# Performance work log

Hardware: AMD Instinct MI355X
Metric: run time of the kernel (lower is better)

The kernel has to match this reference:

```python
import jax, jax.numpy as jnp
import numpy as np

EMBED_DIM = 2048
NUM_HEADS = 16
HEAD_DIM = EMBED_DIM // NUM_HEADS
WINDOW = 512  # window_size; also used as chunk size (S must be a multiple)


def setup_inputs() -> dict:
    key = jax.random.key(0)
    k1, k2, k3 = jax.random.split(key, 3)
    B, S = 2, 4096
    x = jax.random.normal(k1, (B, S, EMBED_DIM), dtype=jnp.float32)
    w_qkv = jax.random.normal(k2, (3 * EMBED_DIM, EMBED_DIM), dtype=jnp.float32) * 0.02
    w_out = jax.random.normal(k3, (EMBED_DIM, EMBED_DIM), dtype=jnp.float32) * 0.02
    return {"x": x, "w_qkv": w_qkv, "w_out": w_out}


def _sliding_window_attn(q, k, v, window):
    # q,k,v: [B,H,S,d]; causal sliding window: kv valid iff 0 <= q_idx - kv_idx <= window.
    # Chunked O(S*window): each query chunk of size C=window attends to its own
    # chunk and the previous one (exactly covers the band of width window+1).
    B, H, S, d = q.shape
    C = window
    nc = S // C
    qc = q.reshape(B, H, nc, C, d)

    def two_chunks(t):
        tc = t.reshape(B, H, nc, C, d)
        prev = jnp.pad(tc[:, :, :-1], ((0, 0), (0, 0), (1, 0), (0, 0), (0, 0)))
        return jnp.concatenate([prev, tc], axis=3)  # [B,H,nc,2C,d]

    kc = two_chunks(k)
    vc = two_chunks(v)

    scale = 1.0 / np.sqrt(d).astype(np.float32)
    scores = jnp.einsum('bhnid,bhnjd->bhnij', qc, kc) * scale  # [B,H,nc,C,2C]

    i = jnp.arange(C)[:, None]            # local query index
    j = jnp.arange(2 * C)[None, :]        # local kv index within the 2-chunk span
    band = (j >= i) & (j <= i + C)        # causal & within window (C == window)
    kv_global = (jnp.arange(nc)[:, None, None] - 1) * C + j[None]  # [nc,1,2C]
    mask = band[None] & (kv_global >= 0)  # [nc,C,2C]; drops padded chunk 0 keys

    scores = jnp.where(mask[None, None], scores, jnp.finfo(scores.dtype).min)
    probs = jax.nn.softmax(scores, axis=-1)
    out = jnp.einsum('bhnij,bhnjd->bhnid', probs, vc)  # [B,H,nc,C,d]
    return out.reshape(B, H, S, d)


def reference(x, w_qkv, w_out):
    B, S, E = x.shape
    qkv = jnp.einsum('bse,fe->bsf', x, w_qkv)                       # [B,S,3E]
    qkv = qkv.reshape(B, S, 3, NUM_HEADS, HEAD_DIM)
    qkv = jnp.transpose(qkv, (2, 0, 3, 1, 4))                        # [3,B,H,S,d]
    q, k, v = qkv[0], qkv[1], qkv[2]
    attn = _sliding_window_attn(q, k, v, WINDOW)                     # [B,H,S,d]
    attn = jnp.transpose(attn, (0, 2, 1, 3)).reshape(B, S, E)
    return jnp.einsum('bse,fe->bsf', attn, w_out)
```

## Files before the change

### kernel.cpp

```cpp
#include <hip/hip_runtime.h>
#include <hip/hip_bf16.h>
#include <math.h>


#define SEQ   4096
#define BATCH 2
#define EMBED 2048
#define HEADS 16
#define HDIM  128
#define NELEM (BATCH * SEQ * EMBED)
#define SCL2E (0.088388347648318447f * 1.4426950408889634f)

typedef __attribute__((ext_vector_type(8))) short short8;
typedef __attribute__((ext_vector_type(4))) float f32x4;

__device__ __forceinline__ unsigned short f2bf(float f) {
    unsigned int u = __float_as_uint(f);
    u = (u + 0x7fff + ((u >> 16) & 1)) >> 16;
    return (unsigned short)u;
}

__device__ __forceinline__ unsigned int cvt_pk_bf16(float a, float b) {
    unsigned int r;
    asm volatile("v_cvt_pk_bf16_f32 %0, %1, %2" : "=v"(r) : "v"(a), "v"(b));
    return r;
}

__global__ void cast3_kernel(const float* __restrict__ x,
                             const float* __restrict__ wq,
                             const float* __restrict__ wo,
                             unsigned short* __restrict__ xb,
                             unsigned short* __restrict__ wqb,
                             unsigned short* __restrict__ wob)
{
    const int nx = NELEM / 8;
    const int nq = 3 * EMBED * EMBED / 8;
    const int no = EMBED * EMBED / 8;
    int i = blockIdx.x * blockDim.x + threadIdx.x;
    const float* s;
    unsigned short* d;
    int j;
    if (i < nx)                { s = x;  d = xb;  j = i; }
    else if (i < nx + nq)      { s = wq; d = wqb; j = i - nx; }
    else if (i < nx + nq + no) { s = wo; d = wob; j = i - nx - nq; }
    else return;
    const float4 v0 = ((const float4*)s)[2 * j];
    const float4 v1 = ((const float4*)s)[2 * j + 1];
    union { unsigned short us[8]; uint4 u4; } o;
    o.us[0] = f2bf(v0.x); o.us[1] = f2bf(v0.y); o.us[2] = f2bf(v0.z); o.us[3] = f2bf(v0.w);
    o.us[4] = f2bf(v1.x); o.us[5] = f2bf(v1.y); o.us[6] = f2bf(v1.z); o.us[7] = f2bf(v1.w);
    ((uint4*)d)[j] = o.u4;
}

template <int MODE>
__global__ __launch_bounds__(512)
void gemm256_kernel(const unsigned short* __restrict__ A,
                    const unsigned short* __restrict__ B,
                    float* __restrict__ C,
                    unsigned short* __restrict__ P0,
                    unsigned short* __restrict__ P1,
                    int M, int N, int K)
{
    __shared__ __align__(16) char lds[131072];

    const int tid  = threadIdx.x;
    const int lane = tid & 63;
    const int w    = tid >> 6;
    const int wm   = w >> 2;
    const int wn   = w & 3;
    const int l16  = lane & 15;
    const int kg   = lane >> 4;

    const int nwg  = gridDim.x * gridDim.y;
    const int bidl = blockIdx.y * gridDim.x + blockIdx.x;
    const int cpx  = nwg >> 3;
    const int swzb = (bidl & 7) * cpx + (bidl >> 3);
    const int m0   = (swzb / gridDim.x) * 256;
    const int n0   = (swzb % gridDim.x) * 256;

    const int srow = w * 8 + (lane >> 3);
    const int sch8 = ((lane & 7) ^ (lane >> 3)) * 8;

    auto stage = [&](const unsigned short* X, int rowbase, int t2, int ldsbase) {
#pragma unroll
        for (int u = 0; u < 2; ++u) {
            const unsigned short* g = X + (size_t)(rowbase + u * 64 + srow) * K
                                      + t2 * 64 + sch8;
            unsigned int lb = __builtin_amdgcn_readfirstlane(
                (unsigned int)(uintptr_t)(lds + ldsbase + u * 8192 + w * 1024));
            asm volatile("s_mov_b32 m0, %0\n\t"
                         "global_load_lds_dwordx4 %1, off"
                         :: "s"(lb), "v"(g) : "memory");
        }
    };
    auto rdA = [&](int p, int mf, int ks) -> short8 {
        return *(const short8*)(lds + p * 32768 + (wm * 128 + mf * 16 + l16) * 128
                                + (((ks * 4 + kg) ^ (l16 & 7)) << 4));
    };
    auto rdB = [&](int p, int nf, int ks) -> short8 {
        return *(const short8*)(lds + 65536 + p * 32768
                                + (wn * 64 + nf * 16 + l16) * 128
                                + (((ks * 4 + kg) ^ (l16 & 7)) << 4));
    };

    f32x4 acc[8][4];
#pragma unroll
    for (int i = 0; i < 8; ++i)
#pragma unroll
        for (int j = 0; j < 4; ++j) acc[i][j] = (f32x4)0.f;

    const int NT = K >> 6;

    stage(A, m0 + 0,   0, 0);
    stage(A, m0 + 128, 0, 16384);
    stage(B, n0 + 0,   0, 65536);
    stage(B, n0 + 128, 0, 65536 + 16384);
    __syncthreads();

    for (int t = 0; t < NT; ++t) {
        const int p = t & 1;
        if (t + 1 < NT) {
            stage(A, m0 + 0,   t + 1, (p ^ 1) * 32768);
            stage(A, m0 + 128, t + 1, (p ^ 1) * 32768 + 16384);
            stage(B, n0 + 0,   t + 1, 65536 + (p ^ 1) * 32768);
            stage(B, n0 + 128, t + 1, 65536 + (p ^ 1) * 32768 + 16384);
        }
        short8 bfr[4][2];
#pragma unroll
        for (int nf = 0; nf < 4; ++nf)
#pragma unroll
            for (int ks = 0; ks < 2; ++ks) bfr[nf][ks] = rdB(p, nf, ks);
#pragma unroll
        for (int mf = 0; mf < 8; ++mf) {
            const short8 a0 = rdA(p, mf, 0);
            const short8 a1 = rdA(p, mf, 1);
#pragma unroll
            for (int nf = 0; nf < 4; ++nf) {
                acc[mf][nf] = __builtin_amdgcn_mfma_f32_16x16x32_bf16(
                    a0, bfr[nf][0], acc[mf][nf], 0, 0, 0);
                acc[mf][nf] = __builtin_amdgcn_mfma_f32_16x16x32_bf16(
                    a1, bfr[nf][1], acc[mf][nf], 0, 0, 0);
            }
        }
        __syncthreads();
    }

    if (MODE == 1) {
        const int cb = n0 + wn * 64;
        unsigned short* dst = (cb >> 11) ? P1 : P0;
        const int h  = (cb >> 7) & 15;
        const int db = cb & 127;
#pragma unroll
        for (int fi = 0; fi < 8; ++fi)
#pragma unroll
            for (int r = 0; r < 4; ++r) {
                const int mrow = m0 + wm * 128 + fi * 16 + kg * 4 + r;
                const int b = mrow >> 12, s = mrow & 4095;
                unsigned short* drow = dst + ((size_t)((b << 4) + h) * SEQ + s) * HDIM
                                       + db + l16;
#pragma unroll
                for (int nf = 0; nf < 4; ++nf) drow[nf * 16] = f2bf(acc[fi][nf][r]);
            }
    } else if (MODE == 2) {
#pragma unroll
        for (int fi = 0; fi < 8; ++fi)
#pragma unroll
            for (int r = 0; r < 4; ++r) {
                const int mrow = m0 + wm * 128 + fi * 16 + kg * 4 + r;
                const int h = mrow >> 7, d = mrow & 127;
#pragma unroll
                for (int nf = 0; nf < 4; ++nf) {
                    const int col = n0 + wn * 64 + nf * 16 + l16;
                    const int b = col >> 12, s = col & 4095;
                    const int sl = s & 63;
                    const int c = (sl & 0x23) | ((sl & 0x0C) << 1) | ((sl & 0x10) >> 2);
                    P0[((size_t)((b << 4) + h) * HDIM + d) * SEQ + (s & ~63) + c] =
                        f2bf(acc[fi][nf][r]);
                }
            }
    } else {
#pragma unroll
        for (int fi = 0; fi < 8; ++fi)
#pragma unroll
            for (int r = 0; r < 4; ++r) {
                float* crow = C + (size_t)(m0 + wm * 128 + fi * 16 + kg * 4 + r) * N
                              + n0 + wn * 64 + l16;
#pragma unroll
                for (int nf = 0; nf < 4; ++nf) crow[nf * 16] = acc[fi][nf][r];
            }
    }
}

__global__ __launch_bounds__(512)
void swa_mfma_kernel(const unsigned short* __restrict__ Qg,
                     const unsigned short* __restrict__ Kg,
                     const unsigned short* __restrict__ Vtg,
                     unsigned short* __restrict__ O )
{
    __shared__ __align__(16) char lds[65536];

    const int bid = blockIdx.x;
    const int qt  = bid & 31;
    const int h   = (bid >> 5) & 15;
    const int b   = bid >> 9;
    const int q0  = qt * 128;
    const int tid  = threadIdx.x;
    const int w    = tid >> 6;
    const int lane = tid & 63;
    const int l16  = lane & 15;
    const int kg   = lane >> 4;
    const size_t base = (size_t)((b << 4) + h) * SEQ * HDIM;
    const int gq = q0 + w * 16 + l16;

    short8 qf[4];
#pragma unroll
    for (int kw = 0; kw < 4; ++kw)
        qf[kw] = *(const short8*)(Qg + base + (size_t)gq * HDIM + kw * 32 + kg * 8);

    f32x4 acc_o[8];
#pragma unroll
    for (int db = 0; db < 8; ++db) acc_o[db] = (f32x4)0.f;
    float m = -1e30f, l = 0.f;

    auto stageKV = [&](int kt, int buf) {
        const int gk0 = q0 - 512 + kt * 64;
#pragma unroll
        for (int u = 0; u < 2; ++u) {
            {
                const int id  = u * 512 + w * 64 + lane;
                const int row = id >> 4, ch = id & 15;
                const char* g = (const char*)(Kg + base + (size_t)(gk0 + row) * HDIM
                                              + ((ch ^ (row & 7)) << 3));
                unsigned int lb = __builtin_amdgcn_readfirstlane(
                    (unsigned int)(uintptr_t)(lds + buf * 32768 + u * 8192 + w * 1024));
                asm volatile("s_mov_b32 m0, %0\n\t"
                             "global_load_lds_dwordx4 %1, off"
                             :: "s"(lb), "v"(g) : "memory");
            }
            {
                const int id  = u * 512 + w * 64 + lane;
                const int d   = id >> 3, ch = id & 7;
                const char* g = (const char*)(Vtg + base + (size_t)d * SEQ + gk0
                                              + ((ch ^ (d & 7)) << 3));
                unsigned int lb = __builtin_amdgcn_readfirstlane(
                    (unsigned int)(uintptr_t)(lds + buf * 32768 + 16384
                                              + u * 8192 + w * 1024));
                asm volatile("s_mov_b32 m0, %0\n\t"
                             "global_load_lds_dwordx4 %1, off"
                             :: "s"(lb), "v"(g) : "memory");
            }
        }
    };

    const int kt_start = (qt < 4) ? (8 - 2 * qt) : 0;
    stageKV(kt_start, 0);
    int cur = 0;

    for (int kt = kt_start; kt < 10; ++kt) {
        asm volatile("s_waitcnt vmcnt(0)" ::: "memory");
        __syncthreads();
        if (kt + 1 < 10) stageKV(kt + 1, cur ^ 1);

        const int gk0 = q0 - 512 + kt * 64;
        const char* ldsb = lds + cur * 32768;
        const int qlo = q0 + w * 16;
        const bool active = (gk0 <= qlo + 15) && (gk0 + 63 >= qlo - 512);
        if (active) {
            const int dqw = qlo - gk0;
            bool kbok[4];
#pragma unroll
            for (int kb = 0; kb < 4; ++kb)
                kbok[kb] = (kb * 16 <= dqw + 15) && (kb * 16 + 15 >= dqw - 512);

            f32x4 s4[4];
#pragma unroll
            for (int kb = 0; kb < 4; ++kb) s4[kb] = (f32x4)0.f;
#pragma unroll
            for (int kb = 0; kb < 4; ++kb) {
                if (kbok[kb]) {
#pragma unroll
                    for (int kw = 0; kw < 4; ++kw) {
                        short8 kf = *(const short8*)(ldsb + (kb * 16 + l16) * 256
                                                     + (((kw * 4 + kg) ^ (l16 & 7)) << 4));
                        s4[kb] = __builtin_amdgcn_mfma_f32_16x16x32_bf16(
                            kf, qf[kw], s4[kb], 0, 0, 0);
                    }
                }
            }

            const int dq = gq - gk0;
            float p[4][4];
            float tm = -1e30f;
#pragma unroll
            for (int kb = 0; kb < 4; ++kb)
#pragma unroll
                for (int r = 0; r < 4; ++r) {
                    const int koff = kb * 16 + kg * 4 + r;
                    const bool valid = (koff <= dq) && (koff >= dq - 512);
                    const float sv = valid ? s4[kb][r] * SCL2E : -1e30f;
                    p[kb][r] = sv;
                    tm = fmaxf(tm, sv);
                }
            tm = fmaxf(tm, __shfl_xor(tm, 16));
            tm = fmaxf(tm, __shfl_xor(tm, 32));
            const float mn   = fmaxf(m, tm);
            const float corr = __builtin_amdgcn_exp2f(m - mn);
            m = mn;
            l *= corr;
            float cr[4];
#pragma unroll
            for (int r = 0; r < 4; ++r) cr[r] = __shfl(corr, kg * 4 + r);
#pragma unroll
            for (int db = 0; db < 8; ++db)
#pragma unroll
                for (int r = 0; r < 4; ++r) acc_o[db][r] *= cr[r];

            float ts = 0.f;
#pragma unroll
            for (int kb = 0; kb < 4; ++kb)
#pragma unroll
                for (int r = 0; r < 4; ++r) {
                    const float pv = (p[kb][r] > -1e29f)
                                         ? __builtin_amdgcn_exp2f(p[kb][r] - m) : 0.f;
                    p[kb][r] = pv;
                    ts += pv;
                }
            ts += __shfl_xor(ts, 16);
            ts += __shfl_xor(ts, 32);
            l += ts;

            unsigned int dw[4][2];
#pragma unroll
            for (int kb = 0; kb < 4; ++kb) {
                dw[kb][0] = cvt_pk_bf16(p[kb][0], p[kb][1]);
                dw[kb][1] = cvt_pk_bf16(p[kb][2], p[kb][3]);
            }
#pragma unroll
            for (int w2 = 0; w2 < 2; ++w2) {
                if (!(kbok[2 * w2] || kbok[2 * w2 + 1])) continue;
                union { unsigned int u[4]; short8 v; } pu;
                pu.u[0] = dw[2 * w2][0];     pu.u[1] = dw[2 * w2][1];
                pu.u[2] = dw[2 * w2 + 1][0]; pu.u[3] = dw[2 * w2 + 1][1];
#pragma unroll
                for (int db = 0; db < 8; ++db) {
                    short8 vf = *(const short8*)(ldsb + 16384 + (db * 16 + l16) * 128
                                                 + (((w2 * 4 + kg) ^ (l16 & 7)) << 4));
                    acc_o[db] = __builtin_amdgcn_mfma_f32_16x16x32_bf16(
                        pu.v, vf, acc_o[db], 0, 0, 0);
                }
            }
        }
        cur ^= 1;
    }

    const float inv = 1.0f / l;
    float li[4];
#pragma unroll
    for (int r = 0; r < 4; ++r) li[r] = __shfl(inv, kg * 4 + r);
#pragma unroll
    for (int db = 0; db < 8; ++db)
#pragma unroll
        for (int r = 0; r < 4; ++r) {
            const int gqr = q0 + w * 16 + kg * 4 + r;
            O[((size_t)b * SEQ + gqr) * EMBED + h * HDIM + db * 16 + l16] =
                f2bf(acc_o[db][r] * li[r]);
        }
}

extern "C" void kernel_launch(void* const* d_in, const int* in_sizes, int n_in,
                              void* d_out, int out_size, void* d_ws, size_t ws_size,
                              hipStream_t stream)
{
    const float* x     = (const float*)d_in[0];
    const float* w_qkv = (const float*)d_in[1];
    const float* w_out = (const float*)d_in[2];
    float* out = (float*)d_out;

    char* ws = (char*)d_ws;
    unsigned short* xb    = (unsigned short*)(ws);
    unsigned short* wqkvb = (unsigned short*)(ws + 33554432);
    unsigned short* woutb = (unsigned short*)(ws + 58720256);
    unsigned short* qb    = (unsigned short*)(ws + 67108864);
    unsigned short* kb    = (unsigned short*)(ws + 100663296);
    unsigned short* vtb   = (unsigned short*)(ws + 134217728);
    unsigned short* attnb = (unsigned short*)(ws + 167772160);

    const int M = BATCH * SEQ;
    dim3 blk(256);

    hipLaunchKernelGGL(cast3_kernel, dim3(16384), blk, 0, stream,
                       x, w_qkv, w_out, xb, wqkvb, woutb);

    hipLaunchKernelGGL((gemm256_kernel<1>), dim3(16, 32), dim3(512), 0, stream,
                       xb, wqkvb, (float*)nullptr, qb, kb, M, 2 * EMBED, EMBED);

    hipLaunchKernelGGL((gemm256_kernel<2>), dim3(32, 8), dim3(512), 0, stream,
                       wqkvb + (size_t)2 * EMBED * EMBED, xb, (float*)nullptr,
                       vtb, (unsigned short*)nullptr, EMBED, M, EMBED);

    hipLaunchKernelGGL(swa_mfma_kernel, dim3(BATCH * HEADS * (SEQ / 128)), dim3(512),
                       0, stream, qb, kb, vtb, attnb);

    hipLaunchKernelGGL((gemm256_kernel<0>), dim3(8, 32), dim3(512), 0, stream,
                       attnb, woutb, out, (unsigned short*)nullptr,
                       (unsigned short*)nullptr, M, EMBED, EMBED);
}
```

Measured before the change: 332.6 us.

## Merge QK and V projection GEMMs into one launch; widen attention tiles to 256 queries

The QK projection and the transposed V projection are merged into a single launch of 768 workgroups, with the block index selecting the mode. This removes one kernel launch and the tail bubble between the two GEMMs. The sliding-window attention kernel now processes 256 queries per block with 1024 threads instead of 128 with 512, so each staged K/V tile is reused by twice as many query rows and the halo overhead shrinks. In exchange there are fewer, larger attention blocks, which can lower occupancy and shorten the pipeline at the sequence start.

```diff
diff --git a/kernel.cpp b/kernel.cpp
--- a/kernel.cpp
+++ b/kernel.cpp
@@ -52,16 +52,15 @@
     ((uint4*)d)[j] = o.u4;
 }
 
-template <int MODE>
 __global__ __launch_bounds__(512)
-void gemm256_kernel(const unsigned short* __restrict__ A,
-                    const unsigned short* __restrict__ B,
-                    float* __restrict__ C,
-                    unsigned short* __restrict__ P0,
-                    unsigned short* __restrict__ P1,
-                    int M, int N, int K)
+void gemm_proj_kernel(const unsigned short* __restrict__ xb,
+                      const unsigned short* __restrict__ wqkvb,
+                      unsigned short* __restrict__ Qo,
+                      unsigned short* __restrict__ Ko,
+                      unsigned short* __restrict__ Vt)
 {
     __shared__ __align__(16) char lds[131072];
+    const int K = EMBED;
 
     const int tid  = threadIdx.x;
     const int lane = tid & 63;
@@ -71,12 +70,18 @@
     const int l16  = lane & 15;
     const int kg   = lane >> 4;
 
-    const int nwg  = gridDim.x * gridDim.y;
-    const int bidl = blockIdx.y * gridDim.x + blockIdx.x;
+    const int blk   = blockIdx.x;
+    const int mode  = (blk < 512) ? 1 : 2;
+    const int bidl  = (mode == 1) ? blk : blk - 512;
+    const int gx    = (mode == 1) ? 16 : 32;
+    const int nwg   = (mode == 1) ? 512 : 256;
+    const unsigned short* A = (mode == 1) ? xb : (wqkvb + (size_t)2 * EMBED * EMBED);
+    const unsigned short* B = (mode == 1) ? wqkvb : xb;
+
     const int cpx  = nwg >> 3;
     const int swzb = (bidl & 7) * cpx + (bidl >> 3);
-    const int m0   = (swzb / gridDim.x) * 256;
-    const int n0   = (swzb % gridDim.x) * 256;
+    const int m0   = (swzb / gx) * 256;
+    const int n0   = (swzb % gx) * 256;
 
     const int srow = w * 8 + (lane >> 3);
     const int sch8 = ((lane & 7) ^ (lane >> 3)) * 8;
@@ -145,9 +150,9 @@
         __syncthreads();
     }
 
-    if (MODE == 1) {
+    if (mode == 1) {
         const int cb = n0 + wn * 64;
-        unsigned short* dst = (cb >> 11) ? P1 : P0;
+        unsigned short* dst = (cb >> 11) ? Ko : Qo;
         const int h  = (cb >> 7) & 15;
         const int db = cb & 127;
 #pragma unroll
@@ -161,7 +166,7 @@
 #pragma unroll
                 for (int nf = 0; nf < 4; ++nf) drow[nf * 16] = f2bf(acc[fi][nf][r]);
             }
-    } else if (MODE == 2) {
+    } else {
 #pragma unroll
         for (int fi = 0; fi < 8; ++fi)
 #pragma unroll
@@ -174,24 +179,115 @@
                     const int b = col >> 12, s = col & 4095;
                     const int sl = s & 63;
                     const int c = (sl & 0x23) | ((sl & 0x0C) << 1) | ((sl & 0x10) >> 2);
-                    P0[((size_t)((b << 4) + h) * HDIM + d) * SEQ + (s & ~63) + c] =
+                    Vt[((size_t)((b << 4) + h) * HDIM + d) * SEQ + (s & ~63) + c] =
                         f2bf(acc[fi][nf][r]);
                 }
             }
-    } else {
-#pragma unroll
-        for (int fi = 0; fi < 8; ++fi)
-#pragma unroll
-            for (int r = 0; r < 4; ++r) {
-                float* crow = C + (size_t)(m0 + wm * 128 + fi * 16 + kg * 4 + r) * N
-                              + n0 + wn * 64 + l16;
-#pragma unroll
-                for (int nf = 0; nf < 4; ++nf) crow[nf * 16] = acc[fi][nf][r];
-            }
     }
 }
 
 __global__ __launch_bounds__(512)
+void gemm_out_kernel(const unsigned short* __restrict__ A,
+                     const unsigned short* __restrict__ B,
+                     float* __restrict__ C,
+                     int M, int N, int K)
+{
+    __shared__ __align__(16) char lds[131072];
+
+    const int tid  = threadIdx.x;
+    const int lane = tid & 63;
+    const int w    = tid >> 6;
+    const int wm   = w >> 2;
+    const int wn   = w & 3;
+    const int l16  = lane & 15;
+    const int kg   = lane >> 4;
+
+    const int nwg  = gridDim.x * gridDim.y;
+    const int bidl = blockIdx.y * gridDim.x + blockIdx.x;
+    const int cpx  = nwg >> 3;
+    const int swzb = (bidl & 7) * cpx + (bidl >> 3);
+    const int m0   = (swzb / gridDim.x) * 256;
+    const int n0   = (swzb % gridDim.x) * 256;
+
+    const int srow = w * 8 + (lane >> 3);
+    const int sch8 = ((lane & 7) ^ (lane >> 3)) * 8;
+
+    auto stage = [&](const unsigned short* X, int rowbase, int t2, int ldsbase) {
+#pragma unroll
+        for (int u = 0; u < 2; ++u) {
+            const unsigned short* g = X + (size_t)(rowbase + u * 64 + srow) * K
+                                      + t2 * 64 + sch8;
+            unsigned int lb = __builtin_amdgcn_readfirstlane(
+                (unsigned int)(uintptr_t)(lds + ldsbase + u * 8192 + w * 1024));
+            asm volatile("s_mov_b32 m0, %0\n\t"
+                         "global_load_lds_dwordx4 %1, off"
+                         :: "s"(lb), "v"(g) : "memory");
+        }
+    };
+    auto rdA = [&](int p, int mf, int ks) -> short8 {
+        return *(const short8*)(lds + p * 32768 + (wm * 128 + mf * 16 + l16) * 128
+                                + (((ks * 4 + kg) ^ (l16 & 7)) << 4));
+    };
+    auto rdB = [&](int p, int nf, int ks) -> short8 {
+        return *(const short8*)(lds + 65536 + p * 32768
+                                + (wn * 64 + nf * 16 + l16) * 128
+                                + (((ks * 4 + kg) ^ (l16 & 7)) << 4));
+    };
+
+    f32x4 acc[8][4];
+#pragma unroll
+    for (int i = 0; i < 8; ++i)
+#pragma unroll
+        for (int j = 0; j < 4; ++j) acc[i][j] = (f32x4)0.f;
+
+    const int NT = K >> 6;
+
+    stage(A, m0 + 0,   0, 0);
+    stage(A, m0 + 128, 0, 16384);
+    stage(B, n0 + 0,   0, 65536);
+    stage(B, n0 + 128, 0, 65536 + 16384);
+    __syncthreads();
+
+    for (int t = 0; t < NT; ++t) {
+        const int p = t & 1;
+        if (t + 1 < NT) {
+            stage(A, m0 + 0,   t + 1, (p ^ 1) * 32768);
+            stage(A, m0 + 128, t + 1, (p ^ 1) * 32768 + 16384);
+            stage(B, n0 + 0,   t + 1, 65536 + (p ^ 1) * 32768);
+            stage(B, n0 + 128, t + 1, 65536 + (p ^ 1) * 32768 + 16384);
+        }
+        short8 bfr[4][2];
+#pragma unroll
+        for (int nf = 0; nf < 4; ++nf)
+#pragma unroll
+            for (int ks = 0; ks < 2; ++ks) bfr[nf][ks] = rdB(p, nf, ks);
+#pragma unroll
+        for (int mf = 0; mf < 8; ++mf) {
+            const short8 a0 = rdA(p, mf, 0);
+            const short8 a1 = rdA(p, mf, 1);
+#pragma unroll
+            for (int nf = 0; nf < 4; ++nf) {
+                acc[mf][nf] = __builtin_amdgcn_mfma_f32_16x16x32_bf16(
+                    a0, bfr[nf][0], acc[mf][nf], 0, 0, 0);
+                acc[mf][nf] = __builtin_amdgcn_mfma_f32_16x16x32_bf16(
+                    a1, bfr[nf][1], acc[mf][nf], 0, 0, 0);
+            }
+        }
+        __syncthreads();
+    }
+
+#pragma unroll
+    for (int fi = 0; fi < 8; ++fi)
+#pragma unroll
+        for (int r = 0; r < 4; ++r) {
+            float* crow = C + (size_t)(m0 + wm * 128 + fi * 16 + kg * 4 + r) * N
+                          + n0 + wn * 64 + l16;
+#pragma unroll
+            for (int nf = 0; nf < 4; ++nf) crow[nf * 16] = acc[fi][nf][r];
+        }
+}
+
+__global__ __launch_bounds__(1024)
 void swa_mfma_kernel(const unsigned short* __restrict__ Qg,
                      const unsigned short* __restrict__ Kg,
                      const unsigned short* __restrict__ Vtg,
@@ -200,10 +296,10 @@
     __shared__ __align__(16) char lds[65536];
 
     const int bid = blockIdx.x;
-    const int qt  = bid & 31;
-    const int h   = (bid >> 5) & 15;
-    const int b   = bid >> 9;
-    const int q0  = qt * 128;
+    const int qt  = bid & 15;
+    const int h   = (bid >> 4) & 15;
+    const int b   = bid >> 8;
+    const int q0  = qt * 256;
     const int tid  = threadIdx.x;
     const int w    = tid >> 6;
     const int lane = tid & 63;
@@ -224,42 +320,36 @@
 
     auto stageKV = [&](int kt, int buf) {
         const int gk0 = q0 - 512 + kt * 64;
-#pragma unroll
-        for (int u = 0; u < 2; ++u) {
-            {
-                const int id  = u * 512 + w * 64 + lane;
-                const int row = id >> 4, ch = id & 15;
-                const char* g = (const char*)(Kg + base + (size_t)(gk0 + row) * HDIM
-                                              + ((ch ^ (row & 7)) << 3));
-                unsigned int lb = __builtin_amdgcn_readfirstlane(
-                    (unsigned int)(uintptr_t)(lds + buf * 32768 + u * 8192 + w * 1024));
-                asm volatile("s_mov_b32 m0, %0\n\t"
-                             "global_load_lds_dwordx4 %1, off"
-                             :: "s"(lb), "v"(g) : "memory");
-            }
-            {
-                const int id  = u * 512 + w * 64 + lane;
-                const int d   = id >> 3, ch = id & 7;
-                const char* g = (const char*)(Vtg + base + (size_t)d * SEQ + gk0
-                                              + ((ch ^ (d & 7)) << 3));
-                unsigned int lb = __builtin_amdgcn_readfirstlane(
-                    (unsigned int)(uintptr_t)(lds + buf * 32768 + 16384
-                                              + u * 8192 + w * 1024));
-                asm volatile("s_mov_b32 m0, %0\n\t"
-                             "global_load_lds_dwordx4 %1, off"
-                             :: "s"(lb), "v"(g) : "memory");
-            }
-        }
-    };
-
-    const int kt_start = (qt < 4) ? (8 - 2 * qt) : 0;
+        {
+            const int row = tid >> 4, ch = tid & 15;
+            const char* g = (const char*)(Kg + base + (size_t)(gk0 + row) * HDIM
+                                          + ((ch ^ (row & 7)) << 3));
+            unsigned int lb = __builtin_amdgcn_readfirstlane(
+                (unsigned int)(uintptr_t)(lds + buf * 32768 + w * 1024));
+            asm volatile("s_mov_b32 m0, %0\n\t"
+                         "global_load_lds_dwordx4 %1, off"
+                         :: "s"(lb), "v"(g) : "memory");
+        }
+        {
+            const int d = tid >> 3, ch = tid & 7;
+            const char* g = (const char*)(Vtg + base + (size_t)d * SEQ + gk0
+                                          + ((ch ^ (d & 7)) << 3));
+            unsigned int lb = __builtin_amdgcn_readfirstlane(
+                (unsigned int)(uintptr_t)(lds + buf * 32768 + 16384 + w * 1024));
+            asm volatile("s_mov_b32 m0, %0\n\t"
+                         "global_load_lds_dwordx4 %1, off"
+                         :: "s"(lb), "v"(g) : "memory");
+        }
+    };
+
+    const int kt_start = (qt < 2) ? (8 - 4 * qt) : 0;
     stageKV(kt_start, 0);
     int cur = 0;
 
-    for (int kt = kt_start; kt < 10; ++kt) {
+    for (int kt = kt_start; kt < 12; ++kt) {
         asm volatile("s_waitcnt vmcnt(0)" ::: "memory");
         __syncthreads();
-        if (kt + 1 < 10) stageKV(kt + 1, cur ^ 1);
+        if (kt + 1 < 12) stageKV(kt + 1, cur ^ 1);
 
         const int gk0 = q0 - 512 + kt * 64;
         const char* ldsb = lds + cur * 32768;
@@ -391,17 +481,12 @@
     hipLaunchKernelGGL(cast3_kernel, dim3(16384), blk, 0, stream,
                        x, w_qkv, w_out, xb, wqkvb, woutb);
 
-    hipLaunchKernelGGL((gemm256_kernel<1>), dim3(16, 32), dim3(512), 0, stream,
-                       xb, wqkvb, (float*)nullptr, qb, kb, M, 2 * EMBED, EMBED);
-
-    hipLaunchKernelGGL((gemm256_kernel<2>), dim3(32, 8), dim3(512), 0, stream,
-                       wqkvb + (size_t)2 * EMBED * EMBED, xb, (float*)nullptr,
-                       vtb, (unsigned short*)nullptr, EMBED, M, EMBED);
-
-    hipLaunchKernelGGL(swa_mfma_kernel, dim3(BATCH * HEADS * (SEQ / 128)), dim3(512),
+    hipLaunchKernelGGL(gemm_proj_kernel, dim3(768), dim3(512), 0, stream,
+                       xb, wqkvb, qb, kb, vtb);
+
+    hipLaunchKernelGGL(swa_mfma_kernel, dim3(BATCH * HEADS * (SEQ / 256)), dim3(1024),
                        0, stream, qb, kb, vtb, attnb);
 
-    hipLaunchKernelGGL((gemm256_kernel<0>), dim3(8, 32), dim3(512), 0, stream,
-                       attnb, woutb, out, (unsigned short*)nullptr,
-                       (unsigned short*)nullptr, M, EMBED, EMBED);
-}
+    hipLaunchKernelGGL(gemm_out_kernel, dim3(8, 32), dim3(512), 0, stream,
+                       attnb, woutb, out, M, EMBED, EMBED);
+}
```

Result: no change. 337.9 us (+1.6%).
